# Kernel tuning notes

Hardware: AMD Instinct MI355X
Metric: run time of the kernel (lower is better)

The kernel has to match this reference:

```python
import jax, jax.numpy as jnp
import numpy as np

D_MODEL = 1024
N_HEADS = 16
HEAD_DIM = D_MODEL // N_HEADS
FOCUS_K = 64
LN_EPS = 1e-5


def setup_inputs() -> dict:
    key = jax.random.key(0)
    ks = jax.random.split(key, 16)
    B, T, N, d = 8, 2048, 32768, D_MODEL
    s = 0.02
    return {
        "h": jax.random.normal(ks[0], (B, T, d), jnp.float32),
        "memory": jax.random.normal(ks[1], (N, d), jnp.float32),
        "activations": jax.random.normal(ks[2], (B, N), jnp.float32),
        "ln_g": jnp.ones((d,), jnp.float32),
        "ln_b": jnp.zeros((d,), jnp.float32),
        "focus_w": jax.random.normal(ks[3], (d, d), jnp.float32) * s,
        "focus_b": jnp.zeros((d,), jnp.float32),
        "qw": jax.random.normal(ks[4], (d, d), jnp.float32) * s,
        "qb": jnp.zeros((d,), jnp.float32),
        "kw": jax.random.normal(ks[5], (d, d), jnp.float32) * s,
        "kb": jnp.zeros((d,), jnp.float32),
        "vw": jax.random.normal(ks[6], (d, d), jnp.float32) * s,
        "vb": jnp.zeros((d,), jnp.float32),
        "ow": jax.random.normal(ks[7], (d, d), jnp.float32) * s,
        "ob": jnp.zeros((d,), jnp.float32),
        "activation_weight": jnp.float32(1.0),
        "gate_logit": jnp.float32(0.0),
    }


def reference(h, memory, activations, ln_g, ln_b, focus_w, focus_b,
              qw, qb, kw, kb, vw, vb, ow, ob, activation_weight, gate_logit):
    B, T, d = h.shape
    N = memory.shape[0]
    K = min(FOCUS_K, N)
    H, Dh = N_HEADS, HEAD_DIM

    # LayerNorm
    mu = h.mean(-1, keepdims=True)
    var = jnp.var(h, axis=-1, keepdims=True)
    h_norm = (h - mu) * jax.lax.rsqrt(var + LN_EPS) * ln_g + ln_b

    # Focus query -> relevance over all N memory slots
    h_summary = h_norm.mean(axis=1)                    # (B, d)
    focus_query = h_summary @ focus_w + focus_b        # (B, d)
    relevance = focus_query @ memory.T                 # (B, N)
    selection = relevance + activation_weight * activations
    _, topk_idx = jax.lax.top_k(selection, K)          # (B, K)

    # Gather K memory vectors per batch
    topk_mem = memory[topk_idx]                        # (B, K, d)

    # Small-K cross-attention
    q = (h_norm @ qw + qb).reshape(B, T, H, Dh).transpose(0, 2, 1, 3)   # (B,H,T,Dh)
    k = (topk_mem @ kw + kb).reshape(B, K, H, Dh).transpose(0, 2, 1, 3)  # (B,H,K,Dh)
    v = (topk_mem @ vw + vb).reshape(B, K, H, Dh).transpose(0, 2, 1, 3)
    scores = jnp.einsum('bhtd,bhkd->bhtk', q, k) / (Dh ** 0.5)
    attn = jax.nn.softmax(scores, axis=-1)             # (B,H,T,K)
    out = jnp.einsum('bhtk,bhkd->bhtd', attn, v)
    out = out.transpose(0, 2, 1, 3).reshape(B, T, d)
    out = out @ ow + ob

    gate = jax.nn.sigmoid(gate_logit)
    h_updated = h + gate * out

    # Scatter mean attention back to full N
    mean_attn_topk = attn.mean(axis=(1, 2))            # (B, K)
    full_attn = jnp.zeros((B, N), h.dtype).at[jnp.arange(B)[:, None], topk_idx].set(mean_attn_topk)
    return h_updated, full_attn
```

## Files before the change

kernel.cpp:

```cpp
#include <hip/hip_runtime.h>

typedef unsigned short u16;
typedef unsigned int u32;
typedef __bf16 bf16x8 __attribute__((ext_vector_type(8)));
typedef float f32x4 __attribute__((ext_vector_type(4)));

#define DM 1024
#define B_ 8
#define T_ 2048
#define NN 32768
#define NH 16
#define DH 64
#define KF 64

__device__ __forceinline__ u16 f2bf(float f) {
  u32 x = __float_as_uint(f);
  x = (x + 0x7fffu + ((x >> 16) & 1u)) >> 16;
  return (u16)x;
}
__device__ __forceinline__ u32 mono(float f) {
  u32 x = __float_as_uint(f);
  return (x & 0x80000000u) ? ~x : (x | 0x80000000u);
}

__global__ void k_zero(float* __restrict__ fullattn, float* __restrict__ colsum,
                       float* __restrict__ mattn) {
  int i = blockIdx.x * 256 + threadIdx.x;
  fullattn[i] = 0.f;
  if (i < B_ * DM) colsum[i] = 0.f;
  if (i < B_ * KF) mattn[i] = 0.f;
}

__global__ __launch_bounds__(256) void k_transpose(
    const float* __restrict__ w0, const float* __restrict__ w1,
    const float* __restrict__ w2, const float* __restrict__ w3,
    u16* __restrict__ o0, u16* __restrict__ o1, u16* __restrict__ o2, u16* __restrict__ o3) {
  __shared__ float t[32][33];
  const float* w = blockIdx.z == 0 ? w0 : blockIdx.z == 1 ? w1 : blockIdx.z == 2 ? w2 : w3;
  u16* o = blockIdx.z == 0 ? o0 : blockIdx.z == 1 ? o1 : blockIdx.z == 2 ? o2 : o3;
  int tx = threadIdx.x & 31, ty = threadIdx.x >> 5;
  int kb = blockIdx.y * 32, nb = blockIdx.x * 32;
#pragma unroll
  for (int j = 0; j < 32; j += 8) t[ty + j][tx] = w[(size_t)(kb + ty + j) * DM + nb + tx];
  __syncthreads();
#pragma unroll
  for (int j = 0; j < 32; j += 8) o[(size_t)(nb + ty + j) * DM + kb + tx] = f2bf(t[tx][ty + j]);
}

__global__ __launch_bounds__(256) void k_ln(const float* __restrict__ h, const float* __restrict__ g,
                                            const float* __restrict__ be, u16* __restrict__ hn,
                                            float* __restrict__ murstd) {
  int r = blockIdx.x, tid = threadIdx.x;
  float4 v = *(const float4*)(h + (size_t)r * DM + tid * 4);
  float s = v.x + v.y + v.z + v.w;
  float q = v.x * v.x + v.y * v.y + v.z * v.z + v.w * v.w;
#pragma unroll
  for (int off = 1; off < 64; off <<= 1) {
    s += __shfl_xor(s, off, 64);
    q += __shfl_xor(q, off, 64);
  }
  __shared__ float rs[4], rq[4];
  int w = tid >> 6;
  if ((tid & 63) == 0) { rs[w] = s; rq[w] = q; }
  __syncthreads();
  s = rs[0] + rs[1] + rs[2] + rs[3];
  q = rq[0] + rq[1] + rq[2] + rq[3];
  float mu = s * (1.f / 1024.f);
  float rstd = rsqrtf(q * (1.f / 1024.f) - mu * mu + 1e-5f);
  float4 gg = *(const float4*)(g + tid * 4);
  float4 bb = *(const float4*)(be + tid * 4);
  float n0 = (v.x - mu) * rstd * gg.x + bb.x;
  float n1 = (v.y - mu) * rstd * gg.y + bb.y;
  float n2 = (v.z - mu) * rstd * gg.z + bb.z;
  float n3 = (v.w - mu) * rstd * gg.w + bb.w;
  uint2 o;
  o.x = (u32)f2bf(n0) | ((u32)f2bf(n1) << 16);
  o.y = (u32)f2bf(n2) | ((u32)f2bf(n3) << 16);
  *(uint2*)(hn + (size_t)r * DM + tid * 4) = o;
  if (tid == 0) { murstd[r * 2] = mu; murstd[r * 2 + 1] = rstd; }
}

__global__ __launch_bounds__(256) void k_summary(const float* __restrict__ h,
                                                 const float* __restrict__ murstd,
                                                 float* __restrict__ colsum) {
  int col = blockIdx.x * 256 + threadIdx.x;
  int b = blockIdx.z;
  int tb = blockIdx.y * 128;
  float acc = 0.f;
  for (int t = 0; t < 128; ++t) {
    int r = b * T_ + tb + t;
    float mu = murstd[r * 2], rsd = murstd[r * 2 + 1];
    acc += (h[(size_t)r * DM + col] - mu) * rsd;
  }
  atomicAdd(&colsum[b * DM + col], acc);
}

__global__ __launch_bounds__(256) void k_focus(const float* __restrict__ colsum,
                                               const float* __restrict__ lng, const float* __restrict__ lnb,
                                               const float* __restrict__ fw, const float* __restrict__ fb,
                                               float* __restrict__ fq) {
  int gid = blockIdx.x * 256 + threadIdx.x;
  int b = gid >> 10, dout = gid & 1023;
  float acc = fb[dout];
  for (int i = 0; i < DM; ++i) {
    float hs = lng[i] * (colsum[b * DM + i] * (1.f / 2048.f)) + lnb[i];
    acc += hs * fw[(size_t)i * DM + dout];
  }
  fq[gid] = acc;
}

__global__ __launch_bounds__(256) void k_selection(const float* __restrict__ mem,
                                                   const float* __restrict__ fqg,
                                                   const float* __restrict__ act,
                                                   const float* __restrict__ awp,
                                                   float* __restrict__ sel) {
  __shared__ float fqs[8][1024];
  int tid = threadIdx.x;
#pragma unroll
  for (int i = 0; i < 8; ++i) {
    int e = i * 256 + tid;
    ((float4*)&fqs[0][0])[e] = ((const float4*)fqg)[e];
  }
  __syncthreads();
  float aw = awp[0];
  int l = tid & 63, w = tid >> 6;
  for (int n = blockIdx.x * 4 + w; n < NN; n += gridDim.x * 4) {
    const float* mrow = mem + (size_t)n * DM;
    float accb[8] = {0, 0, 0, 0, 0, 0, 0, 0};
#pragma unroll
    for (int c = 0; c < 4; ++c) {
      int d = c * 256 + l * 4;
      float4 mv = *(const float4*)(mrow + d);
#pragma unroll
      for (int b2 = 0; b2 < 8; ++b2) {
        float4 fv = *(const float4*)&fqs[b2][d];
        accb[b2] += mv.x * fv.x + mv.y * fv.y + mv.z * fv.z + mv.w * fv.w;
      }
    }
#pragma unroll
    for (int off = 1; off < 64; off <<= 1) {
#pragma unroll
      for (int b2 = 0; b2 < 8; ++b2) accb[b2] += __shfl_xor(accb[b2], off, 64);
    }
    if (l < 8) {
      float vsel = accb[0];
#pragma unroll
      for (int j = 1; j < 8; ++j) vsel = (l == j) ? accb[j] : vsel;
      sel[(size_t)l * NN + n] = vsel + aw * act[(size_t)l * NN + n];
    }
  }
}

#define CAND 1024
__global__ __launch_bounds__(1024) void k_topk(const float* __restrict__ sel, int* __restrict__ idx) {
  int b = blockIdx.x, tid = threadIdx.x;
  __shared__ u32 hist[256], hist2[256];
  __shared__ int scb, sA, ssb, sA2, nDef, nCand;
  __shared__ u32 cu[CAND];
  __shared__ int cn[CAND];
  __shared__ unsigned long long amax;
  if (tid < 256) { hist[tid] = 0; hist2[tid] = 0; }
  if (tid == 0) { nDef = 0; nCand = 0; }
  __syncthreads();
  const float* row = sel + (size_t)b * NN;
  for (int i = tid; i < NN; i += 1024) atomicAdd(&hist[mono(row[i]) >> 24], 1u);
  __syncthreads();
  if (tid < 256) {
    u32 s = 0;
    for (int j = tid + 1; j < 256; ++j) s += hist[j];
    if ((int)s < KF && (int)(s + hist[tid]) >= KF) { scb = tid; sA = (int)s; }
  }
  __syncthreads();
  int cb = scb;
  int R = KF - sA;
  for (int i = tid; i < NN; i += 1024) {
    u32 u = mono(row[i]);
    if ((int)(u >> 24) == cb) atomicAdd(&hist2[(u >> 16) & 255], 1u);
  }
  __syncthreads();
  if (tid < 256) {
    u32 s = 0;
    for (int j = tid + 1; j < 256; ++j) s += hist2[j];
    if ((int)s < R && (int)(s + hist2[tid]) >= R) { ssb = tid; sA2 = (int)s; }
  }
  __syncthreads();
  int R2 = R - sA2;
  u32 T16 = ((u32)cb << 8) | (u32)ssb;
  for (int i = tid; i < NN; i += 1024) {
    u32 u = mono(row[i]);
    u32 t = u >> 16;
    if (t > T16) {
      int p = atomicAdd(&nDef, 1);
      idx[b * KF + p] = i;
    } else if (t == T16) {
      int p = atomicAdd(&nCand, 1);
      if (p < CAND) { cu[p] = u; cn[p] = i; }
    }
  }
  __syncthreads();
  int base = nDef;
  int nc = nCand < CAND ? nCand : CAND;
  for (int r = 0; r < R2; ++r) {
    if (tid == 0) amax = 0;
    __syncthreads();
    unsigned long long loc = 0;
    for (int i = tid; i < nc; i += 1024) {
      unsigned long long key = ((unsigned long long)cu[i] << 32) | (u32)i;
      if (key > loc) loc = key;
    }
    if (loc) atomicMax(&amax, loc);
    __syncthreads();
    if (tid == 0) {
      int pos = (int)(amax & 0xffffffffu);
      idx[b * KF + base + r] = cn[pos];
      cu[pos] = 0;
    }
    __syncthreads();
  }
}

__global__ __launch_bounds__(256) void k_gather(const float* __restrict__ mem,
                                                const int* __restrict__ idx, u16* __restrict__ tm) {
  int rowi = blockIdx.x;
  int n = idx[rowi];
  float4 v = ((const float4*)(mem + (size_t)n * DM))[threadIdx.x];
  uint2 o;
  o.x = (u32)f2bf(v.x) | ((u32)f2bf(v.y) << 16);
  o.y = (u32)f2bf(v.z) | ((u32)f2bf(v.w) << 16);
  *(uint2*)(tm + (size_t)rowi * DM + threadIdx.x * 4) = o;
}

__global__ __launch_bounds__(256) void k_gemm(const u16* __restrict__ A, const u16* __restrict__ Bt,
                                              const float* __restrict__ bias, void* __restrict__ out,
                                              const float* __restrict__ hsrc, const float* __restrict__ gatep,
                                              int M, int N, int K, int mode) {
  __shared__ u16 As[128][40];
  __shared__ u16 Bs[128][40];
  int tid = threadIdx.x;
  int l = tid & 63, w = tid >> 6;
  int l15 = l & 15, quad = l >> 4;
  int wm = w >> 1, wn = w & 1;
  int m0 = blockIdx.y * 128, n0 = blockIdx.x * 128;
  int srow = tid >> 1, sseg = (tid & 1) * 16;
  const u16* ga = A + (size_t)(m0 + srow) * K + sseg;
  const u16* gb = Bt + (size_t)(n0 + srow) * K + sseg;
  f32x4 zero = {0.f, 0.f, 0.f, 0.f};
  f32x4 acc[4][4];
#pragma unroll
  for (int mt = 0; mt < 4; ++mt)
#pragma unroll
    for (int nt = 0; nt < 4; ++nt) acc[mt][nt] = zero;
  for (int kt = 0; kt < K; kt += 32) {
    uint4 a0 = *(const uint4*)(ga + kt);
    uint4 a1 = *(const uint4*)(ga + kt + 8);
    uint4 b0 = *(const uint4*)(gb + kt);
    uint4 b1 = *(const uint4*)(gb + kt + 8);
    __syncthreads();
    *(uint4*)&As[srow][sseg] = a0;
    *(uint4*)&As[srow][sseg + 8] = a1;
    *(uint4*)&Bs[srow][sseg] = b0;
    *(uint4*)&Bs[srow][sseg + 8] = b1;
    __syncthreads();
    bf16x8 af[4], bfr[4];
#pragma unroll
    for (int t = 0; t < 4; ++t) {
      af[t] = *(const bf16x8*)&As[wm * 64 + t * 16 + l15][quad * 8];
      bfr[t] = *(const bf16x8*)&Bs[wn * 64 + t * 16 + l15][quad * 8];
    }
#pragma unroll
    for (int mt = 0; mt < 4; ++mt)
#pragma unroll
      for (int nt = 0; nt < 4; ++nt)
        acc[mt][nt] = __builtin_amdgcn_mfma_f32_16x16x32_bf16(af[mt], bfr[nt], acc[mt][nt], 0, 0, 0);
  }
  float gv = 0.f;
  if (mode == 1) gv = 1.f / (1.f + __expf(-gatep[0]));
#pragma unroll
  for (int mt = 0; mt < 4; ++mt) {
#pragma unroll
    for (int nt = 0; nt < 4; ++nt) {
      int col = n0 + wn * 64 + nt * 16 + l15;
      float bv = bias[col];
#pragma unroll
      for (int reg = 0; reg < 4; ++reg) {
        int rrow = m0 + wm * 64 + mt * 16 + quad * 4 + reg;
        float v = acc[mt][nt][reg] + bv;
        if (mode == 0) {
          ((u16*)out)[(size_t)rrow * N + col] = f2bf(v);
        } else if (mode == 1) {
          size_t o = (size_t)rrow * N + col;
          ((float*)out)[o] = hsrc[o] + gv * v;
        } else {
          int bb = rrow >> 6, ks = rrow & 63, hh = col >> 6, dh = col & 63;
          size_t o;
          if (mode == 2) o = ((((size_t)bb * NH + hh) * KF + ks) * DH + dh);
          else o = ((((size_t)bb * NH + hh) * DH + dh) * KF + ks);
          ((u16*)out)[o] = f2bf(v);
        }
      }
    }
  }
}

__global__ __launch_bounds__(256) void k_attn(const u16* __restrict__ q, const u16* __restrict__ kk,
                                              const u16* __restrict__ vt, u16* __restrict__ o,
                                              float* __restrict__ mattn) {
  __shared__ u16 Qs[128][72];
  __shared__ u16 Ps[128][72];
  __shared__ u16 Ks[64][72];
  __shared__ u16 Vs[64][72];
  int tid = threadIdx.x;
  int t0 = blockIdx.x * 128, hh = blockIdx.y, b = blockIdx.z;
  {
    int row = tid >> 1, seg = tid & 1;
    const uint4* src = (const uint4*)(q + ((size_t)(b * T_ + t0 + row)) * DM + hh * DH + seg * 32);
#pragma unroll
    for (int j = 0; j < 4; ++j) *(uint4*)&Qs[row][seg * 32 + j * 8] = src[j];
  }
  {
    int row = tid >> 2, seg = tid & 3;
    size_t base = (((size_t)b * NH + hh) * 64 + row) * 64 + seg * 16;
    const uint4* sk = (const uint4*)(kk + base);
    const uint4* sv = (const uint4*)(vt + base);
    *(uint4*)&Ks[row][seg * 16] = sk[0];
    *(uint4*)&Ks[row][seg * 16 + 8] = sk[1];
    *(uint4*)&Vs[row][seg * 16] = sv[0];
    *(uint4*)&Vs[row][seg * 16 + 8] = sv[1];
  }
  __syncthreads();
  int l = tid & 63, w = tid >> 6;
  int l15 = l & 15, quad = l >> 4;
  f32x4 zero = {0.f, 0.f, 0.f, 0.f};
  f32x4 sacc[2][4];
#pragma unroll
  for (int mt = 0; mt < 2; ++mt)
#pragma unroll
    for (int nt = 0; nt < 4; ++nt) sacc[mt][nt] = zero;
#pragma unroll
  for (int step = 0; step < 2; ++step) {
    bf16x8 aq0 = *(const bf16x8*)&Qs[w * 32 + l15][step * 32 + quad * 8];
    bf16x8 aq1 = *(const bf16x8*)&Qs[w * 32 + 16 + l15][step * 32 + quad * 8];
#pragma unroll
    for (int nt = 0; nt < 4; ++nt) {
      bf16x8 bk = *(const bf16x8*)&Ks[nt * 16 + l15][step * 32 + quad * 8];
      sacc[0][nt] = __builtin_amdgcn_mfma_f32_16x16x32_bf16(aq0, bk, sacc[0][nt], 0, 0, 0);
      sacc[1][nt] = __builtin_amdgcn_mfma_f32_16x16x32_bf16(aq1, bk, sacc[1][nt], 0, 0, 0);
    }
  }
  float csum[4] = {0, 0, 0, 0};
#pragma unroll
  for (int mt = 0; mt < 2; ++mt) {
#pragma unroll
    for (int reg = 0; reg < 4; ++reg) {
      float s0 = sacc[mt][0][reg] * 0.125f;
      float s1 = sacc[mt][1][reg] * 0.125f;
      float s2 = sacc[mt][2][reg] * 0.125f;
      float s3 = sacc[mt][3][reg] * 0.125f;
      float mx = fmaxf(fmaxf(s0, s1), fmaxf(s2, s3));
#pragma unroll
      for (int off = 1; off < 16; off <<= 1) mx = fmaxf(mx, __shfl_xor(mx, off, 64));
      float p0 = __expf(s0 - mx), p1 = __expf(s1 - mx), p2 = __expf(s2 - mx), p3 = __expf(s3 - mx);
      float sum = p0 + p1 + p2 + p3;
#pragma unroll
      for (int off = 1; off < 16; off <<= 1) sum += __shfl_xor(sum, off, 64);
      float inv = 1.f / sum;
      p0 *= inv; p1 *= inv; p2 *= inv; p3 *= inv;
      int row = w * 32 + mt * 16 + quad * 4 + reg;
      Ps[row][0 * 16 + l15] = f2bf(p0);
      Ps[row][1 * 16 + l15] = f2bf(p1);
      Ps[row][2 * 16 + l15] = f2bf(p2);
      Ps[row][3 * 16 + l15] = f2bf(p3);
      csum[0] += p0; csum[1] += p1; csum[2] += p2; csum[3] += p3;
    }
  }
#pragma unroll
  for (int nt = 0; nt < 4; ++nt) {
    float v = csum[nt];
    v += __shfl_xor(v, 16, 64);
    v += __shfl_xor(v, 32, 64);
    if (quad == 0) atomicAdd(&mattn[b * KF + nt * 16 + l15], v);
  }
  __syncthreads();
  f32x4 oacc[2][4];
#pragma unroll
  for (int mt = 0; mt < 2; ++mt)
#pragma unroll
    for (int nt = 0; nt < 4; ++nt) oacc[mt][nt] = zero;
#pragma unroll
  for (int step = 0; step < 2; ++step) {
    bf16x8 ap0 = *(const bf16x8*)&Ps[w * 32 + l15][step * 32 + quad * 8];
    bf16x8 ap1 = *(const bf16x8*)&Ps[w * 32 + 16 + l15][step * 32 + quad * 8];
#pragma unroll
    for (int nt = 0; nt < 4; ++nt) {
      bf16x8 bv = *(const bf16x8*)&Vs[nt * 16 + l15][step * 32 + quad * 8];
      oacc[0][nt] = __builtin_amdgcn_mfma_f32_16x16x32_bf16(ap0, bv, oacc[0][nt], 0, 0, 0);
      oacc[1][nt] = __builtin_amdgcn_mfma_f32_16x16x32_bf16(ap1, bv, oacc[1][nt], 0, 0, 0);
    }
  }
#pragma unroll
  for (int mt = 0; mt < 2; ++mt)
#pragma unroll
    for (int nt = 0; nt < 4; ++nt)
#pragma unroll
      for (int reg = 0; reg < 4; ++reg) {
        int row = t0 + w * 32 + mt * 16 + quad * 4 + reg;
        int col = hh * DH + nt * 16 + l15;
        o[((size_t)(b * T_ + row)) * DM + col] = f2bf(oacc[mt][nt][reg]);
      }
}

__global__ void k_scatter(const float* __restrict__ mattn, const int* __restrict__ tidx,
                          float* __restrict__ out_attn) {
  int i = threadIdx.x;
  int b = i >> 6;
  out_attn[(size_t)b * NN + tidx[i]] = mattn[i] * (1.f / 32768.f);
}

extern "C" void kernel_launch(void* const* d_in, const int* in_sizes, int n_in,
                              void* d_out, int out_size, void* d_ws, size_t ws_size,
                              hipStream_t stream) {
  const float* h = (const float*)d_in[0];
  const float* mem = (const float*)d_in[1];
  const float* act = (const float*)d_in[2];
  const float* lng = (const float*)d_in[3];
  const float* lnb = (const float*)d_in[4];
  const float* fw = (const float*)d_in[5];
  const float* fb = (const float*)d_in[6];
  const float* qw = (const float*)d_in[7];
  const float* qb = (const float*)d_in[8];
  const float* kw = (const float*)d_in[9];
  const float* kb = (const float*)d_in[10];
  const float* vw = (const float*)d_in[11];
  const float* vb = (const float*)d_in[12];
  const float* ow = (const float*)d_in[13];
  const float* ob = (const float*)d_in[14];
  const float* awp = (const float*)d_in[15];
  const float* glp = (const float*)d_in[16];
  float* out_h = (float*)d_out;
  float* out_attn = out_h + (size_t)B_ * T_ * DM;

  char* p = (char*)d_ws;
  size_t off = 0;
  auto take = [&](size_t bytes) {
    void* r = p + off;
    off += (bytes + 255) & ~(size_t)255;
    return r;
  };
  u16* hnorm = (u16*)take((size_t)B_ * T_ * DM * 2);
  u16* q_ws = (u16*)take((size_t)B_ * T_ * DM * 2);
  u16* qwT = (u16*)take((size_t)DM * DM * 2);
  u16* kwT = (u16*)take((size_t)DM * DM * 2);
  u16* vwT = (u16*)take((size_t)DM * DM * 2);
  u16* owT = (u16*)take((size_t)DM * DM * 2);
  float* selw = (float*)take((size_t)B_ * NN * 4);
  u16* tmem = (u16*)take((size_t)B_ * KF * DM * 2);
  u16* k_ws = (u16*)take((size_t)B_ * NH * KF * DH * 2);
  u16* vT_ws = (u16*)take((size_t)B_ * NH * KF * DH * 2);
  float* murstd = (float*)take((size_t)B_ * T_ * 2 * 4);
  float* colsum = (float*)take((size_t)B_ * DM * 4);
  float* fq = (float*)take((size_t)B_ * DM * 4);
  float* mattn = (float*)take((size_t)B_ * KF * 4);
  int* tidx = (int*)take((size_t)B_ * KF * 4);
  u16* o_ws = hnorm;

  k_zero<<<1024, 256, 0, stream>>>(out_attn, colsum, mattn);
  k_transpose<<<dim3(32, 32, 4), 256, 0, stream>>>(qw, kw, vw, ow, qwT, kwT, vwT, owT);
  k_ln<<<B_ * T_, 256, 0, stream>>>(h, lng, lnb, hnorm, murstd);
  k_gemm<<<dim3(8, 128), 256, 0, stream>>>(hnorm, qwT, qb, q_ws, nullptr, nullptr, B_ * T_, DM, DM, 0);
  k_summary<<<dim3(4, 16, 8), 256, 0, stream>>>(h, murstd, colsum);
  k_focus<<<32, 256, 0, stream>>>(colsum, lng, lnb, fw, fb, fq);
  k_selection<<<2048, 256, 0, stream>>>(mem, fq, act, awp, selw);
  k_topk<<<8, 1024, 0, stream>>>(selw, tidx);
  k_gather<<<B_ * KF, 256, 0, stream>>>(mem, tidx, tmem);
  k_gemm<<<dim3(8, 4), 256, 0, stream>>>(tmem, kwT, kb, k_ws, nullptr, nullptr, B_ * KF, DM, DM, 2);
  k_gemm<<<dim3(8, 4), 256, 0, stream>>>(tmem, vwT, vb, vT_ws, nullptr, nullptr, B_ * KF, DM, DM, 3);
  k_attn<<<dim3(16, 16, 8), 256, 0, stream>>>(q_ws, k_ws, vT_ws, o_ws, mattn);
  k_gemm<<<dim3(8, 128), 256, 0, stream>>>(o_ws, owT, ob, out_h, h, glp, B_ * T_, DM, DM, 1);
  k_scatter<<<1, 512, 0, stream>>>(mattn, tidx, out_attn);
}
```

Baseline: 766.5 us.

## Load GEMM tiles directly into LDS asynchronously and swap grid raster order

The bf16 GEMM now stages A and B tiles with global_load_lds 16-byte direct-to-LDS loads instead of loading into registers and storing to shared memory. To fit the per-wave contiguous write pattern, the LDS tiles drop their row padding and become dense 32-element rows. The grid is also transposed so the M tiles run along blockIdx.x, which makes neighbouring blocks share the same weight tile. The unpadded layout may cause LDS bank conflicts on the MFMA fragment reads, and there is still no double-buffering to overlap the loads with compute.

New measurement: 735.0 us. 4.1% less time.

```diff
diff --git a/kernel.cpp b/kernel.cpp
--- a/kernel.cpp
+++ b/kernel.cpp
@@ -21,6 +21,10 @@
 __device__ __forceinline__ u32 mono(float f) {
   u32 x = __float_as_uint(f);
   return (x & 0x80000000u) ? ~x : (x | 0x80000000u);
+}
+__device__ __forceinline__ void async16(const void* g, void* s) {
+  __builtin_amdgcn_global_load_lds((const __attribute__((address_space(1))) void*)g,
+                                   (__attribute__((address_space(3))) void*)s, 16, 0, 0);
 }
 
 __global__ void k_zero(float* __restrict__ fullattn, float* __restrict__ colsum,
@@ -234,16 +238,22 @@
                                               const float* __restrict__ bias, void* __restrict__ out,
                                               const float* __restrict__ hsrc, const float* __restrict__ gatep,
                                               int M, int N, int K, int mode) {
-  __shared__ u16 As[128][40];
-  __shared__ u16 Bs[128][40];
+  __shared__ __align__(16) u16 As[128 * 32];
+  __shared__ __align__(16) u16 Bs[128 * 32];
   int tid = threadIdx.x;
   int l = tid & 63, w = tid >> 6;
   int l15 = l & 15, quad = l >> 4;
   int wm = w >> 1, wn = w & 1;
-  int m0 = blockIdx.y * 128, n0 = blockIdx.x * 128;
-  int srow = tid >> 1, sseg = (tid & 1) * 16;
-  const u16* ga = A + (size_t)(m0 + srow) * K + sseg;
-  const u16* gb = Bt + (size_t)(n0 + srow) * K + sseg;
+  int m0 = blockIdx.x * 128, n0 = blockIdx.y * 128;
+  int srow = w * 16 + (l >> 2);
+  int koff = (l & 3) * 8;
+  const u16* ga = A + (size_t)(m0 + srow) * K + koff;
+  const u16* gb = Bt + (size_t)(n0 + srow) * K + koff;
+  u16* lA0 = &As[(w * 16) * 32];
+  u16* lA1 = &As[(64 + w * 16) * 32];
+  u16* lB0 = &Bs[(w * 16) * 32];
+  u16* lB1 = &Bs[(64 + w * 16) * 32];
+  size_t rstride = (size_t)64 * K;
   f32x4 zero = {0.f, 0.f, 0.f, 0.f};
   f32x4 acc[4][4];
 #pragma unroll
@@ -251,21 +261,17 @@
 #pragma unroll
     for (int nt = 0; nt < 4; ++nt) acc[mt][nt] = zero;
   for (int kt = 0; kt < K; kt += 32) {
-    uint4 a0 = *(const uint4*)(ga + kt);
-    uint4 a1 = *(const uint4*)(ga + kt + 8);
-    uint4 b0 = *(const uint4*)(gb + kt);
-    uint4 b1 = *(const uint4*)(gb + kt + 8);
     __syncthreads();
-    *(uint4*)&As[srow][sseg] = a0;
-    *(uint4*)&As[srow][sseg + 8] = a1;
-    *(uint4*)&Bs[srow][sseg] = b0;
-    *(uint4*)&Bs[srow][sseg + 8] = b1;
+    async16(ga + kt, lA0);
+    async16(ga + rstride + kt, lA1);
+    async16(gb + kt, lB0);
+    async16(gb + rstride + kt, lB1);
     __syncthreads();
     bf16x8 af[4], bfr[4];
 #pragma unroll
     for (int t = 0; t < 4; ++t) {
-      af[t] = *(const bf16x8*)&As[wm * 64 + t * 16 + l15][quad * 8];
-      bfr[t] = *(const bf16x8*)&Bs[wn * 64 + t * 16 + l15][quad * 8];
+      af[t] = *(const bf16x8*)&As[(wm * 64 + t * 16 + l15) * 32 + quad * 8];
+      bfr[t] = *(const bf16x8*)&Bs[(wn * 64 + t * 16 + l15) * 32 + quad * 8];
     }
 #pragma unroll
     for (int mt = 0; mt < 4; ++mt)
@@ -466,15 +472,15 @@
   k_zero<<<1024, 256, 0, stream>>>(out_attn, colsum, mattn);
   k_transpose<<<dim3(32, 32, 4), 256, 0, stream>>>(qw, kw, vw, ow, qwT, kwT, vwT, owT);
   k_ln<<<B_ * T_, 256, 0, stream>>>(h, lng, lnb, hnorm, murstd);
-  k_gemm<<<dim3(8, 128), 256, 0, stream>>>(hnorm, qwT, qb, q_ws, nullptr, nullptr, B_ * T_, DM, DM, 0);
+  k_gemm<<<dim3(128, 8), 256, 0, stream>>>(hnorm, qwT, qb, q_ws, nullptr, nullptr, B_ * T_, DM, DM, 0);
   k_summary<<<dim3(4, 16, 8), 256, 0, stream>>>(h, murstd, colsum);
   k_focus<<<32, 256, 0, stream>>>(colsum, lng, lnb, fw, fb, fq);
   k_selection<<<2048, 256, 0, stream>>>(mem, fq, act, awp, selw);
   k_topk<<<8, 1024, 0, stream>>>(selw, tidx);
   k_gather<<<B_ * KF, 256, 0, stream>>>(mem, tidx, tmem);
-  k_gemm<<<dim3(8, 4), 256, 0, stream>>>(tmem, kwT, kb, k_ws, nullptr, nullptr, B_ * KF, DM, DM, 2);
-  k_gemm<<<dim3(8, 4), 256, 0, stream>>>(tmem, vwT, vb, vT_ws, nullptr, nullptr, B_ * KF, DM, DM, 3);
+  k_gemm<<<dim3(4, 8), 256, 0, stream>>>(tmem, kwT, kb, k_ws, nullptr, nullptr, B_ * KF, DM, DM, 2);
+  k_gemm<<<dim3(4, 8), 256, 0, stream>>>(tmem, vwT, vb, vT_ws, nullptr, nullptr, B_ * KF, DM, DM, 3);
   k_attn<<<dim3(16, 16, 8), 256, 0, stream>>>(q_ws, k_ws, vT_ws, o_ws, mattn);
-  k_gemm<<<dim3(8, 128), 256, 0, stream>>>(o_ws, owT, ob, out_h, h, glp, B_ * T_, DM, DM, 1);
+  k_gemm<<<dim3(128, 8), 256, 0, stream>>>(o_ws, owT, ob, out_h, h, glp, B_ * T_, DM, DM, 1);
   k_scatter<<<1, 512, 0, stream>>>(mattn, tidx, out_attn);
 }
```
